# Optimization experiments

Measured on AMD Instinct MI355X. Metric: run time of the kernel, lower is better.

## Reference

```python
import jax, jax.numpy as jnp
import numpy as np

COMMITMENT_COST = 0.25


def setup_inputs() -> dict:
    key = jax.random.key(0)
    k1, k2 = jax.random.split(key)
    B, S, D, K = 64, 512, 512, 4096
    inputs = jax.random.normal(k1, (B, S, D), dtype=jnp.float32)
    # codebook initialized uniform(-1/K, 1/K) like the torch module
    codebook = jax.random.uniform(k2, (K, D), dtype=jnp.float32,
                                  minval=-1.0 / K, maxval=1.0 / K)
    return {"inputs": inputs, "codebook": codebook}


def reference(inputs, codebook):
    D = inputs.shape[-1]
    flat = inputs.reshape(-1, D)  # [N, D]
    # squared euclidean distances to every code: [N, K]
    dist = (jnp.sum(flat * flat, axis=1, keepdims=True)
            + jnp.sum(codebook * codebook, axis=1)
            - 2.0 * flat @ codebook.T)
    idx = jnp.argmin(dist, axis=1)  # [N]
    # gather replaces one-hot scatter + matmul (same math)
    quantized = codebook[idx].reshape(inputs.shape)
    commitment_loss = jnp.mean((jax.lax.stop_gradient(quantized) - inputs) ** 2)
    codebook_loss = jnp.mean((quantized - jax.lax.stop_gradient(inputs)) ** 2)
    quantize_loss = COMMITMENT_COST * commitment_loss + codebook_loss
    # straight-through estimator
    quantized_st = inputs + jax.lax.stop_gradient(quantized - inputs)
    encoding_indices = idx.reshape(inputs.shape[:-1])
    return quantized_st, quantize_loss, encoding_indices
```

## Files before the change

### kernel.cpp

```cpp
#include <hip/hip_runtime.h>

#define N_ROWS 32768
#define DIM    512
#define KCODES 4096
#define NPARTS 4
#define KPART  (KCODES / NPARTS)
#define Q_ELEMS (N_ROWS * DIM)
#define LOSS_OFF Q_ELEMS
#define IDX_OFF (Q_ELEMS + 1)

__global__ void k_cnorm(const float* __restrict__ cb, float* __restrict__ cnorm) {
    int wave = (blockIdx.x * blockDim.x + threadIdx.x) >> 6;
    int lane = threadIdx.x & 63;
    if (wave >= KCODES) return;
    const float4* row = (const float4*)(cb + (size_t)wave * DIM);
    float4 v1 = row[lane];
    float4 v2 = row[lane + 64];
    float s = v1.x*v1.x + v1.y*v1.y + v1.z*v1.z + v1.w*v1.w
            + v2.x*v2.x + v2.y*v2.y + v2.z*v2.z + v2.w*v2.w;
    #pragma unroll
    for (int m = 32; m >= 1; m >>= 1) s += __shfl_xor(s, m);
    if (lane == 0) cnorm[wave] = s;
}

__global__ void k_xnorm(const float* __restrict__ x, float* __restrict__ xnorm) {
    int wave = (blockIdx.x * blockDim.x + threadIdx.x) >> 6;
    int lane = threadIdx.x & 63;
    if (wave >= N_ROWS) return;
    const float4* row = (const float4*)(x + (size_t)wave * DIM);
    float4 v1 = row[lane];
    float4 v2 = row[lane + 64];
    float s = v1.x*v1.x + v1.y*v1.y + v1.z*v1.z + v1.w*v1.w
            + v2.x*v2.x + v2.y*v2.y + v2.z*v2.z + v2.w*v2.w;
    #pragma unroll
    for (int m = 32; m >= 1; m >>= 1) s += __shfl_xor(s, m);
    if (lane == 0) xnorm[wave] = s;
}

#define BM 64
#define BN 128
#define BD 32
#define NTHR 128
#define NCH ((KPART / BN) * (DIM / BD))

__global__ __launch_bounds__(NTHR)
void k_argmin(const float* __restrict__ x, const float* __restrict__ cb,
              const float* __restrict__ cnorm, const float* __restrict__ xnorm,
              float* __restrict__ bestv, int* __restrict__ bestk) {
    __shared__ float xs[BM][BD + 4];
    __shared__ float cs[BD][BN];

    const int tid = threadIdx.x;
    const int ty = tid >> 4;
    const int tx = tid & 15;
    const int r0 = blockIdx.x * BM;
    const int kbase = blockIdx.y * KPART;

    float xn[8];
    #pragma unroll
    for (int i = 0; i < 8; ++i) xn[i] = xnorm[r0 + ty + 8 * i];

    float best[8];
    int   bidx[8];
    #pragma unroll
    for (int i = 0; i < 8; ++i) { best[i] = 3.4e38f; bidx[i] = kbase; }

    float acc[8][8];

    #pragma unroll 1
    for (int it = 0; it < NCH; ++it) {
        const int kc = it >> 4;
        const int dc = (it & 15) * BD;

        __syncthreads();
        #pragma unroll
        for (int s = 0; s < 4; ++s) {
            int f = tid + s * NTHR;
            int row = f >> 3;
            int dq  = f & 7;
            *(float4*)&xs[row][dq * 4] =
                *(const float4*)(x + (size_t)(r0 + row) * DIM + dc + dq * 4);
        }
        {
            const float* crow = cb + (size_t)(kbase + kc * BN + tid) * DIM + dc;
            #pragma unroll
            for (int dq = 0; dq < 8; ++dq) {
                float4 v = *(const float4*)(crow + dq * 4);
                cs[dq * 4 + 0][tid] = v.x;
                cs[dq * 4 + 1][tid] = v.y;
                cs[dq * 4 + 2][tid] = v.z;
                cs[dq * 4 + 3][tid] = v.w;
            }
        }
        __syncthreads();

        if ((it & 15) == 0) {
            #pragma unroll
            for (int i = 0; i < 8; ++i)
                #pragma unroll
                for (int j = 0; j < 8; ++j) acc[i][j] = 0.f;
        }

        #pragma unroll
        for (int d4 = 0; d4 < 8; ++d4) {
            float4 xa[8];
            #pragma unroll
            for (int i = 0; i < 8; ++i)
                xa[i] = *(const float4*)&xs[ty + 8 * i][d4 * 4];
            #pragma unroll
            for (int dd = 0; dd < 4; ++dd) {
                int d = d4 * 4 + dd;
                float4 b0 = *(const float4*)&cs[d][tx * 4];
                float4 b1 = *(const float4*)&cs[d][64 + tx * 4];
                #pragma unroll
                for (int i = 0; i < 8; ++i) {
                    float a = (dd == 0) ? xa[i].x : (dd == 1) ? xa[i].y
                            : (dd == 2) ? xa[i].z : xa[i].w;
                    acc[i][0] = fmaf(a, b0.x, acc[i][0]);
                    acc[i][1] = fmaf(a, b0.y, acc[i][1]);
                    acc[i][2] = fmaf(a, b0.z, acc[i][2]);
                    acc[i][3] = fmaf(a, b0.w, acc[i][3]);
                    acc[i][4] = fmaf(a, b1.x, acc[i][4]);
                    acc[i][5] = fmaf(a, b1.y, acc[i][5]);
                    acc[i][6] = fmaf(a, b1.z, acc[i][6]);
                    acc[i][7] = fmaf(a, b1.w, acc[i][7]);
                }
            }
        }

        if ((it & 15) == 15) {
            #pragma unroll
            for (int half = 0; half < 2; ++half) {
                #pragma unroll
                for (int j = 0; j < 4; ++j) {
                    int k = kbase + kc * BN + half * 64 + tx * 4 + j;
                    float cn = cnorm[k];
                    #pragma unroll
                    for (int i = 0; i < 8; ++i) {
                        float t1 = xn[i] + cn;
                        float tw = 2.0f * acc[i][half * 4 + j];
                        float s  = t1 - tw;
                        if (s < best[i]) { best[i] = s; bidx[i] = k; }
                    }
                }
            }
        }
    }

    #pragma unroll
    for (int i = 0; i < 8; ++i) {
        float b = best[i];
        int   ix = bidx[i];
        #pragma unroll
        for (int m = 1; m <= 8; m <<= 1) {
            float ob = __shfl_xor(b, m);
            int   oi = __shfl_xor(ix, m);
            if (ob < b || (ob == b && oi < ix)) { b = ob; ix = oi; }
        }
        if (tx == 0) {
            int row = r0 + ty + 8 * i;
            bestv[(size_t)blockIdx.y * N_ROWS + row] = b;
            bestk[(size_t)blockIdx.y * N_ROWS + row] = ix;
        }
    }
}

__global__ void k_gather(const float* __restrict__ x, const float* __restrict__ cb,
                         const float* __restrict__ bestv, const int* __restrict__ bestk,
                         float* __restrict__ qout, float* __restrict__ idx_out,
                         float* __restrict__ partial) {
    int row  = blockIdx.x * 4 + (threadIdx.x >> 6);
    int lane = threadIdx.x & 63;
    float bv = bestv[row];
    int   bk = bestk[row];
    #pragma unroll
    for (int p = 1; p < NPARTS; ++p) {
        float v = bestv[(size_t)p * N_ROWS + row];
        int   kk = bestk[(size_t)p * N_ROWS + row];
        if (v < bv) { bv = v; bk = kk; }
    }
    if (lane == 0) idx_out[row] = (float)bk;
    const float4* crow = (const float4*)(cb + (size_t)bk * DIM);
    const float4* xrow = (const float4*)(x + (size_t)row * DIM);
    float4* qrow = (float4*)(qout + (size_t)row * DIM);
    float s = 0.f;
    #pragma unroll
    for (int it = 0; it < 2; ++it) {
        int d4 = lane + it * 64;
        float4 q = crow[d4];
        float4 xi = xrow[d4];
        qrow[d4] = q;
        float dx = q.x - xi.x; s += dx * dx;
        dx = q.y - xi.y; s += dx * dx;
        dx = q.z - xi.z; s += dx * dx;
        dx = q.w - xi.w; s += dx * dx;
    }
    #pragma unroll
    for (int m = 32; m >= 1; m >>= 1) s += __shfl_xor(s, m);
    __shared__ float ws4[4];
    if (lane == 0) ws4[threadIdx.x >> 6] = s;
    __syncthreads();
    if (threadIdx.x == 0)
        partial[blockIdx.x] = (ws4[0] + ws4[1]) + (ws4[2] + ws4[3]);
}

__global__ void k_loss(const float* __restrict__ partial, float* __restrict__ out_loss) {
    int t = threadIdx.x;
    double s = 0.0;
    #pragma unroll 4
    for (int i = 0; i < 32; ++i) s += (double)partial[t * 32 + i];
    #pragma unroll
    for (int m = 32; m >= 1; m >>= 1) s += __shfl_xor(s, m);
    __shared__ double sd[4];
    if ((t & 63) == 0) sd[t >> 6] = s;
    __syncthreads();
    if (t == 0) {
        double tot = (sd[0] + sd[1]) + (sd[2] + sd[3]);
        out_loss[0] = (float)(1.25 * tot / (double)Q_ELEMS);
    }
}

extern "C" void kernel_launch(void* const* d_in, const int* in_sizes, int n_in,
                              void* d_out, int out_size, void* d_ws, size_t ws_size,
                              hipStream_t stream) {
    const float* x  = (const float*)d_in[0];
    const float* cb = (const float*)d_in[1];
    float* out = (float*)d_out;

    char* ws = (char*)d_ws;
    float* cnorm = (float*)ws;                      ws += (size_t)KCODES * 4;
    float* xnorm = (float*)ws;                      ws += (size_t)N_ROWS * 4;
    float* bestv = (float*)ws;                      ws += (size_t)NPARTS * N_ROWS * 4;
    int*   bestk = (int*)ws;                        ws += (size_t)NPARTS * N_ROWS * 4;
    float* part  = (float*)ws;

    k_cnorm<<<KCODES / 4, 256, 0, stream>>>(cb, cnorm);
    k_xnorm<<<N_ROWS / 4, 256, 0, stream>>>(x, xnorm);
    dim3 agrid(N_ROWS / BM, NPARTS);
    k_argmin<<<agrid, NTHR, 0, stream>>>(x, cb, cnorm, xnorm, bestv, bestk);
    k_gather<<<N_ROWS / 4, 256, 0, stream>>>(x, cb, bestv, bestk, out, out + IDX_OFF, part);
    k_loss<<<1, 256, 0, stream>>>(part, out + LOSS_OFF);
}
```

Before: 1.968 ms.

## Enlarge argmin tile to 128 rows, split codes 8 ways, merge via 64-bit atomicMin

Doubles the row tile per block (256 threads, 128 rows) so each codebook chunk loaded into shared memory is reused across more rows. It also splits the codebook into 8 partitions instead of 4 to keep the grid size up. Per-partition results are merged with a packed, order-preserving (distance, index) 64-bit atomicMin instead of separate arrays reduced in the gather kernel. The cost is an extra init kernel and atomic traffic. The larger tile may also lower occupancy, since the x tile in shared memory grows.

After: 1.701 ms. 13.6% less time.

```diff
diff --git a/kernel.cpp b/kernel.cpp
--- a/kernel.cpp
+++ b/kernel.cpp
@@ -3,11 +3,16 @@
 #define N_ROWS 32768
 #define DIM    512
 #define KCODES 4096
-#define NPARTS 4
+#define NPARTS 8
 #define KPART  (KCODES / NPARTS)
 #define Q_ELEMS (N_ROWS * DIM)
 #define LOSS_OFF Q_ELEMS
 #define IDX_OFF (Q_ELEMS + 1)
+
+__global__ void k_init(unsigned long long* __restrict__ bk) {
+    int i = blockIdx.x * blockDim.x + threadIdx.x;
+    if (i < N_ROWS) bk[i] = 0xFFFFFFFFFFFFFFFFull;
+}
 
 __global__ void k_cnorm(const float* __restrict__ cb, float* __restrict__ cnorm) {
     int wave = (blockIdx.x * blockDim.x + threadIdx.x) >> 6;
@@ -37,16 +42,16 @@
     if (lane == 0) xnorm[wave] = s;
 }
 
-#define BM 64
+#define BM 128
 #define BN 128
 #define BD 32
-#define NTHR 128
+#define NTHR 256
 #define NCH ((KPART / BN) * (DIM / BD))
 
 __global__ __launch_bounds__(NTHR)
 void k_argmin(const float* __restrict__ x, const float* __restrict__ cb,
               const float* __restrict__ cnorm, const float* __restrict__ xnorm,
-              float* __restrict__ bestv, int* __restrict__ bestk) {
+              unsigned long long* __restrict__ bestkey) {
     __shared__ float xs[BM][BD + 4];
     __shared__ float cs[BD][BN];
 
@@ -56,9 +61,12 @@
     const int r0 = blockIdx.x * BM;
     const int kbase = blockIdx.y * KPART;
 
+    const int ck   = tid & 127;
+    const int cdq0 = tid >> 7;
+
     float xn[8];
     #pragma unroll
-    for (int i = 0; i < 8; ++i) xn[i] = xnorm[r0 + ty + 8 * i];
+    for (int i = 0; i < 8; ++i) xn[i] = xnorm[r0 + ty + 16 * i];
 
     float best[8];
     int   bidx[8];
@@ -81,16 +89,14 @@
             *(float4*)&xs[row][dq * 4] =
                 *(const float4*)(x + (size_t)(r0 + row) * DIM + dc + dq * 4);
         }
-        {
-            const float* crow = cb + (size_t)(kbase + kc * BN + tid) * DIM + dc;
-            #pragma unroll
-            for (int dq = 0; dq < 8; ++dq) {
-                float4 v = *(const float4*)(crow + dq * 4);
-                cs[dq * 4 + 0][tid] = v.x;
-                cs[dq * 4 + 1][tid] = v.y;
-                cs[dq * 4 + 2][tid] = v.z;
-                cs[dq * 4 + 3][tid] = v.w;
-            }
+        #pragma unroll
+        for (int it2 = 0; it2 < 4; ++it2) {
+            int dq = cdq0 + it2 * 2;
+            float4 v = *(const float4*)(cb + (size_t)(kbase + kc * BN + ck) * DIM + dc + dq * 4);
+            cs[dq * 4 + 0][ck] = v.x;
+            cs[dq * 4 + 1][ck] = v.y;
+            cs[dq * 4 + 2][ck] = v.z;
+            cs[dq * 4 + 3][ck] = v.w;
         }
         __syncthreads();
 
@@ -106,7 +112,7 @@
             float4 xa[8];
             #pragma unroll
             for (int i = 0; i < 8; ++i)
-                xa[i] = *(const float4*)&xs[ty + 8 * i][d4 * 4];
+                xa[i] = *(const float4*)&xs[ty + 16 * i][d4 * 4];
             #pragma unroll
             for (int dd = 0; dd < 4; ++dd) {
                 int d = d4 * 4 + dd;
@@ -158,27 +164,22 @@
             if (ob < b || (ob == b && oi < ix)) { b = ob; ix = oi; }
         }
         if (tx == 0) {
-            int row = r0 + ty + 8 * i;
-            bestv[(size_t)blockIdx.y * N_ROWS + row] = b;
-            bestk[(size_t)blockIdx.y * N_ROWS + row] = ix;
+            int row = r0 + ty + 16 * i;
+            unsigned int ub = __float_as_uint(b);
+            ub = (ub & 0x80000000u) ? ~ub : (ub | 0x80000000u);
+            unsigned long long key = ((unsigned long long)ub << 32) | (unsigned int)ix;
+            atomicMin(bestkey + row, key);
         }
     }
 }
 
 __global__ void k_gather(const float* __restrict__ x, const float* __restrict__ cb,
-                         const float* __restrict__ bestv, const int* __restrict__ bestk,
+                         const unsigned long long* __restrict__ bestkey,
                          float* __restrict__ qout, float* __restrict__ idx_out,
                          float* __restrict__ partial) {
     int row  = blockIdx.x * 4 + (threadIdx.x >> 6);
     int lane = threadIdx.x & 63;
-    float bv = bestv[row];
-    int   bk = bestk[row];
-    #pragma unroll
-    for (int p = 1; p < NPARTS; ++p) {
-        float v = bestv[(size_t)p * N_ROWS + row];
-        int   kk = bestk[(size_t)p * N_ROWS + row];
-        if (v < bv) { bv = v; bk = kk; }
-    }
+    int bk = (int)(bestkey[row] & 0xFFFFFFFFull);
     if (lane == 0) idx_out[row] = (float)bk;
     const float4* crow = (const float4*)(cb + (size_t)bk * DIM);
     const float4* xrow = (const float4*)(x + (size_t)row * DIM);
@@ -228,16 +229,16 @@
     float* out = (float*)d_out;
 
     char* ws = (char*)d_ws;
-    float* cnorm = (float*)ws;                      ws += (size_t)KCODES * 4;
-    float* xnorm = (float*)ws;                      ws += (size_t)N_ROWS * 4;
-    float* bestv = (float*)ws;                      ws += (size_t)NPARTS * N_ROWS * 4;
-    int*   bestk = (int*)ws;                        ws += (size_t)NPARTS * N_ROWS * 4;
+    unsigned long long* bestkey = (unsigned long long*)ws;  ws += (size_t)N_ROWS * 8;
+    float* cnorm = (float*)ws;                              ws += (size_t)KCODES * 4;
+    float* xnorm = (float*)ws;                              ws += (size_t)N_ROWS * 4;
     float* part  = (float*)ws;
 
+    k_init<<<N_ROWS / 256, 256, 0, stream>>>(bestkey);
     k_cnorm<<<KCODES / 4, 256, 0, stream>>>(cb, cnorm);
     k_xnorm<<<N_ROWS / 4, 256, 0, stream>>>(x, xnorm);
     dim3 agrid(N_ROWS / BM, NPARTS);
-    k_argmin<<<agrid, NTHR, 0, stream>>>(x, cb, cnorm, xnorm, bestv, bestk);
-    k_gather<<<N_ROWS / 4, 256, 0, stream>>>(x, cb, bestv, bestk, out, out + IDX_OFF, part);
+    k_argmin<<<agrid, NTHR, 0, stream>>>(x, cb, cnorm, xnorm, bestkey);
+    k_gather<<<N_ROWS / 4, 256, 0, stream>>>(x, cb, bestkey, out, out + IDX_OFF, part);
     k_loss<<<1, 256, 0, stream>>>(part, out + LOSS_OFF);
 }
```
